# Kernel tuning notes

Measured on AMD Instinct MI355X. Metric: run time of the kernel, lower is better.

## Reference

```python
import jax, jax.numpy as jnp
import numpy as np

EPS = 1e-05
RFN = 0.5  # blend factor between group-norm path and per-token layer-norm path


def _ln_last(x, eps):
    # layer_norm over last dim, no affine (matches F.layer_norm(x, x.shape[-1:]))
    mu = jnp.mean(x, axis=-1, keepdims=True)
    var = jnp.mean(jnp.square(x - mu), axis=-1, keepdims=True)
    return (x - mu) * jax.lax.rsqrt(var + eps)


def setup_inputs() -> dict:
    key = jax.random.key(0)
    kx, kw, kb = jax.random.split(key, 3)
    B, T, D, G = 8, 4000, 1024, 5
    x = jax.random.normal(kx, (B, T, D), dtype=jnp.float32)
    mask = jnp.ones((G, T // G), dtype=jnp.int32)  # default dense mask: 5 contiguous groups
    weight = jax.random.normal(kw, (D,), dtype=jnp.float32)
    bias = jax.random.normal(kb, (D,), dtype=jnp.float32)
    return {"x": x, "mask": mask, "weight": weight, "bias": bias}


def reference(x, mask, weight, bias):
    B, T, D = x.shape
    G = mask.shape[0]          # number of groups from mask rows
    L = T // G                 # tokens per group (dense ones mask => contiguous blocks)

    # rfn_mode == 'in': per-token layer norm over feature dim
    lned = _ln_last(x, EPS)

    # per-group layer norm over (group_tokens, features) jointly, matching
    # F.layer_norm(x[:, i], normalized_shape=x[:, i].shape[-2:])
    xg = x.reshape(B, G, L, D)
    mu = jnp.mean(xg, axis=(-2, -1), keepdims=True)
    var = jnp.mean(jnp.square(xg - mu), axis=(-2, -1), keepdims=True)
    gn = ((xg - mu) * jax.lax.rsqrt(var + EPS)).reshape(B, T, D)

    return (RFN * gn + (1.0 - RFN) * lned) * weight + bias
```

## Files before the change

kernel.cpp:

```cpp
#include <hip/hip_runtime.h>


#define EPS 1e-5f
#define NUM_G 5
#define CHUNKS_PER_GROUP 32

__global__ __launch_bounds__(256) void group_stats_kernel(
    const float4* __restrict__ x, float* __restrict__ gstats,
    int vec4_per_group) {
  const int group = blockIdx.x / CHUNKS_PER_GROUP;
  const int chunk = blockIdx.x % CHUNKS_PER_GROUP;
  const int per_chunk = vec4_per_group / CHUNKS_PER_GROUP;
  const long base = (long)group * vec4_per_group + (long)chunk * per_chunk;

  float s = 0.f, sq = 0.f;
  for (int i = threadIdx.x; i < per_chunk; i += 256) {
    float4 v = x[base + i];
    s  += (v.x + v.y) + (v.z + v.w);
    sq += (v.x * v.x + v.y * v.y) + (v.z * v.z + v.w * v.w);
  }
  #pragma unroll
  for (int off = 32; off > 0; off >>= 1) {
    s  += __shfl_down(s,  off, 64);
    sq += __shfl_down(sq, off, 64);
  }
  __shared__ float ls[4], lq[4];
  const int wave = threadIdx.x >> 6, lane = threadIdx.x & 63;
  if (lane == 0) { ls[wave] = s; lq[wave] = sq; }
  __syncthreads();
  if (threadIdx.x == 0) {
    float ts = (ls[0] + ls[1]) + (ls[2] + ls[3]);
    float tq = (lq[0] + lq[1]) + (lq[2] + lq[3]);
    atomicAdd(&gstats[2 * group + 0], ts);
    atomicAdd(&gstats[2 * group + 1], tq);
  }
}

__global__ __launch_bounds__(256) void rfnorm_out_kernel(
    const float4* __restrict__ x, const float* __restrict__ gstats,
    const float4* __restrict__ weight, const float4* __restrict__ bias,
    float4* __restrict__ out, int T, int L, float invD, float invNg) {
  const int row = blockIdx.x;
  const int t = row % T;
  const int b = row / T;
  const int group = b * NUM_G + (t / L);
  const long base = (long)row * 256;

  float4 v = x[base + threadIdx.x];
  float s  = (v.x + v.y) + (v.z + v.w);
  float sq = (v.x * v.x + v.y * v.y) + (v.z * v.z + v.w * v.w);
  #pragma unroll
  for (int off = 32; off > 0; off >>= 1) {
    s  += __shfl_down(s,  off, 64);
    sq += __shfl_down(sq, off, 64);
  }
  __shared__ float ls[4], lq[4];
  const int wave = threadIdx.x >> 6, lane = threadIdx.x & 63;
  if (lane == 0) { ls[wave] = s; lq[wave] = sq; }
  __syncthreads();
  const float ts = (ls[0] + ls[1]) + (ls[2] + ls[3]);
  const float tq = (lq[0] + lq[1]) + (lq[2] + lq[3]);

  const float tmu  = ts * invD;
  const float tvar = tq * invD - tmu * tmu;
  const float trs  = rsqrtf(tvar + EPS) * 0.5f;

  const float gsum = gstats[2 * group + 0];
  const float gsq  = gstats[2 * group + 1];
  const float gmu  = gsum * invNg;
  const float gvar = gsq * invNg - gmu * gmu;
  const float grs  = rsqrtf(gvar + EPS) * 0.5f;

  const float4 w  = weight[threadIdx.x];
  const float4 bb = bias[threadIdx.x];

  float4 o;
  o.x = ((v.x - gmu) * grs + (v.x - tmu) * trs) * w.x + bb.x;
  o.y = ((v.y - gmu) * grs + (v.y - tmu) * trs) * w.y + bb.y;
  o.z = ((v.z - gmu) * grs + (v.z - tmu) * trs) * w.z + bb.z;
  o.w = ((v.w - gmu) * grs + (v.w - tmu) * trs) * w.w + bb.w;
  out[base + threadIdx.x] = o;
}

extern "C" void kernel_launch(void* const* d_in, const int* in_sizes, int n_in,
                              void* d_out, int out_size, void* d_ws, size_t ws_size,
                              hipStream_t stream) {
  const float* x      = (const float*)d_in[0];
  const float* weight = (const float*)d_in[2];
  const float* bias   = (const float*)d_in[3];
  float* out          = (float*)d_out;
  float* gstats       = (float*)d_ws;

  const int D = in_sizes[2];
  const int T = in_sizes[1];
  const int B = in_sizes[0] / (T * D);
  const int L = T / NUM_G;
  const long Ng = (long)L * D;
  const int vec4_per_group = (int)(Ng / 4);

  hipMemsetAsync(gstats, 0, (size_t)(B * NUM_G * 2) * sizeof(float), stream);

  dim3 blk(256);
  dim3 grid1(B * NUM_G * CHUNKS_PER_GROUP);
  group_stats_kernel<<<grid1, blk, 0, stream>>>(
      (const float4*)x, gstats, vec4_per_group);

  dim3 grid2(B * T);
  rfnorm_out_kernel<<<grid2, blk, 0, stream>>>(
      (const float4*)x, gstats, (const float4*)weight, (const float4*)bias,
      (float4*)out, T, L, 1.0f / D, 1.0f / (float)Ng);
}
```

Baseline: 258.7 us.

## Compute per-token stats in the stats pass and process four rows per block

Moves the per-token mean and rstd computation into the first pass, with one wave per row, and writes them to a small workspace buffer. The output kernel no longer needs reductions or a block barrier and handles four rows per block. This removes the shuffle and syncthreads work from the second pass and cuts the block count by four. In exchange, the stats kernel now issues one atomic pair per block, about 8000 blocks instead of 1280, and the group index comes from row/L, which assumes groups never straddle a 4-row block.

```diff
diff --git a/kernel.cpp b/kernel.cpp
--- a/kernel.cpp
+++ b/kernel.cpp
@@ -3,83 +3,77 @@
 
 #define EPS 1e-5f
 #define NUM_G 5
-#define CHUNKS_PER_GROUP 32
 
-__global__ __launch_bounds__(256) void group_stats_kernel(
+#define GSTATS_FLOATS 128
+
+__global__ __launch_bounds__(256) void stats_kernel(
     const float4* __restrict__ x, float* __restrict__ gstats,
-    int vec4_per_group) {
-  const int group = blockIdx.x / CHUNKS_PER_GROUP;
-  const int chunk = blockIdx.x % CHUNKS_PER_GROUP;
-  const int per_chunk = vec4_per_group / CHUNKS_PER_GROUP;
-  const long base = (long)group * vec4_per_group + (long)chunk * per_chunk;
+    float2* __restrict__ tstats, int L, float invD) {
+  const int wave = threadIdx.x >> 6, lane = threadIdx.x & 63;
+  const int row = blockIdx.x * 4 + wave;
+  const long base = (long)row * 256;
 
   float s = 0.f, sq = 0.f;
-  for (int i = threadIdx.x; i < per_chunk; i += 256) {
-    float4 v = x[base + i];
+  #pragma unroll
+  for (int j = 0; j < 4; ++j) {
+    float4 v = x[base + lane + 64 * j];
     s  += (v.x + v.y) + (v.z + v.w);
     sq += (v.x * v.x + v.y * v.y) + (v.z * v.z + v.w * v.w);
   }
   #pragma unroll
-  for (int off = 32; off > 0; off >>= 1) {
-    s  += __shfl_down(s,  off, 64);
-    sq += __shfl_down(sq, off, 64);
+  for (int off = 1; off < 64; off <<= 1) {
+    s  += __shfl_xor(s,  off, 64);
+    sq += __shfl_xor(sq, off, 64);
   }
   __shared__ float ls[4], lq[4];
-  const int wave = threadIdx.x >> 6, lane = threadIdx.x & 63;
-  if (lane == 0) { ls[wave] = s; lq[wave] = sq; }
+  if (lane == 0) {
+    const float tmu  = s * invD;
+    const float tvar = sq * invD - tmu * tmu;
+    float2 st;
+    st.x = tmu;
+    st.y = rsqrtf(tvar + EPS) * 0.5f;
+    tstats[row] = st;
+    ls[wave] = s;
+    lq[wave] = sq;
+  }
   __syncthreads();
   if (threadIdx.x == 0) {
-    float ts = (ls[0] + ls[1]) + (ls[2] + ls[3]);
-    float tq = (lq[0] + lq[1]) + (lq[2] + lq[3]);
-    atomicAdd(&gstats[2 * group + 0], ts);
-    atomicAdd(&gstats[2 * group + 1], tq);
+    const int group = row / L;
+    atomicAdd(&gstats[2 * group + 0], (ls[0] + ls[1]) + (ls[2] + ls[3]));
+    atomicAdd(&gstats[2 * group + 1], (lq[0] + lq[1]) + (lq[2] + lq[3]));
   }
 }
 
-__global__ __launch_bounds__(256) void rfnorm_out_kernel(
+__global__ __launch_bounds__(256) void out_kernel(
     const float4* __restrict__ x, const float* __restrict__ gstats,
+    const float2* __restrict__ tstats,
     const float4* __restrict__ weight, const float4* __restrict__ bias,
-    float4* __restrict__ out, int T, int L, float invD, float invNg) {
-  const int row = blockIdx.x;
-  const int t = row % T;
-  const int b = row / T;
-  const int group = b * NUM_G + (t / L);
-  const long base = (long)row * 256;
+    float4* __restrict__ out, int L, float invNg) {
+  const int tid = threadIdx.x;
+  const float4 w  = weight[tid];
+  const float4 bb = bias[tid];
+  const int row0 = blockIdx.x * 4;
 
-  float4 v = x[base + threadIdx.x];
-  float s  = (v.x + v.y) + (v.z + v.w);
-  float sq = (v.x * v.x + v.y * v.y) + (v.z * v.z + v.w * v.w);
   #pragma unroll
-  for (int off = 32; off > 0; off >>= 1) {
-    s  += __shfl_down(s,  off, 64);
-    sq += __shfl_down(sq, off, 64);
+  for (int r = 0; r < 4; ++r) {
+    const int row = row0 + r;
+    const int group = row / L;
+    const float gs = gstats[2 * group + 0];
+    const float gq = gstats[2 * group + 1];
+    const float gmu = gs * invNg;
+    const float grs = rsqrtf(gq * invNg - gmu * gmu + EPS) * 0.5f;
+    const float2 st = tstats[row];
+    const float tmu = st.x, trs = st.y;
+
+    const long base = (long)row * 256;
+    const float4 v = x[base + tid];
+    float4 o;
+    o.x = ((v.x - gmu) * grs + (v.x - tmu) * trs) * w.x + bb.x;
+    o.y = ((v.y - gmu) * grs + (v.y - tmu) * trs) * w.y + bb.y;
+    o.z = ((v.z - gmu) * grs + (v.z - tmu) * trs) * w.z + bb.z;
+    o.w = ((v.w - gmu) * grs + (v.w - tmu) * trs) * w.w + bb.w;
+    out[base + tid] = o;
   }
-  __shared__ float ls[4], lq[4];
-  const int wave = threadIdx.x >> 6, lane = threadIdx.x & 63;
-  if (lane == 0) { ls[wave] = s; lq[wave] = sq; }
-  __syncthreads();
-  const float ts = (ls[0] + ls[1]) + (ls[2] + ls[3]);
-  const float tq = (lq[0] + lq[1]) + (lq[2] + lq[3]);
-
-  const float tmu  = ts * invD;
-  const float tvar = tq * invD - tmu * tmu;
-  const float trs  = rsqrtf(tvar + EPS) * 0.5f;
-
-  const float gsum = gstats[2 * group + 0];
-  const float gsq  = gstats[2 * group + 1];
-  const float gmu  = gsum * invNg;
-  const float gvar = gsq * invNg - gmu * gmu;
-  const float grs  = rsqrtf(gvar + EPS) * 0.5f;
-
-  const float4 w  = weight[threadIdx.x];
-  const float4 bb = bias[threadIdx.x];
-
-  float4 o;
-  o.x = ((v.x - gmu) * grs + (v.x - tmu) * trs) * w.x + bb.x;
-  o.y = ((v.y - gmu) * grs + (v.y - tmu) * trs) * w.y + bb.y;
-  o.z = ((v.z - gmu) * grs + (v.z - tmu) * trs) * w.z + bb.z;
-  o.w = ((v.w - gmu) * grs + (v.w - tmu) * trs) * w.w + bb.w;
-  out[base + threadIdx.x] = o;
 }
 
 extern "C" void kernel_launch(void* const* d_in, const int* in_sizes, int n_in,
@@ -90,23 +84,23 @@
   const float* bias   = (const float*)d_in[3];
   float* out          = (float*)d_out;
   float* gstats       = (float*)d_ws;
+  float2* tstats      = (float2*)((float*)d_ws + GSTATS_FLOATS);
 
   const int D = in_sizes[2];
   const int T = in_sizes[1];
   const int B = in_sizes[0] / (T * D);
   const int L = T / NUM_G;
   const long Ng = (long)L * D;
-  const int vec4_per_group = (int)(Ng / 4);
+  const int n_rows = B * T;
 
   hipMemsetAsync(gstats, 0, (size_t)(B * NUM_G * 2) * sizeof(float), stream);
 
   dim3 blk(256);
-  dim3 grid1(B * NUM_G * CHUNKS_PER_GROUP);
-  group_stats_kernel<<<grid1, blk, 0, stream>>>(
-      (const float4*)x, gstats, vec4_per_group);
+  stats_kernel<<<dim3(n_rows / 4), blk, 0, stream>>>(
+      (const float4*)x, gstats, tstats, L, 1.0f / D);
 
-  dim3 grid2(B * T);
-  rfnorm_out_kernel<<<grid2, blk, 0, stream>>>(
-      (const float4*)x, gstats, (const float4*)weight, (const float4*)bias,
-      (float4*)out, T, L, 1.0f / D, 1.0f / (float)Ng);
+  out_kernel<<<dim3(n_rows / 4), blk, 0, stream>>>(
+      (const float4*)x, gstats, tstats,
+      (const float4*)weight, (const float4*)bias,
+      (float4*)out, L, 1.0f / (float)Ng);
 }
```

Result: slower. 319.7 us (+23.6%).
